# Performance work log

Measured on AMD Instinct MI355X. Metric: run time of the kernel, lower is better.

The kernel has to match this reference:

```python
import math
import jax, jax.numpy as jnp
import numpy as np

B, T, C = 4, 2048, 2048
LAYER_ID, N_LAYER = 12, 24


def setup_inputs() -> dict:
    key = jax.random.key(0)
    kx, kk, kv, kr, ko = jax.random.split(key, 5)
    x = jax.random.normal(kx, (B, T, C), dtype=jnp.float32)

    # parameter init faithful to the torch __init__
    ratio_1_to_almost0 = 1.0 - LAYER_ID / N_LAYER
    ratio_0_to_1 = LAYER_ID / (N_LAYER - 1)
    h = np.arange(C, dtype=np.float64)
    zigzag = (((np.arange(C) + 1) % 3) - 1) * 0.5
    time_first = jnp.asarray(np.ones(C) * math.log(0.3) + zigzag, dtype=jnp.float32)
    base = (h / C)  # x[0,0,i] = i / n_embed
    time_mix_k = jnp.asarray((base ** ratio_1_to_almost0)[None, None, :], dtype=jnp.float32)
    time_mix_v = jnp.asarray((base ** ratio_1_to_almost0 + 0.3 * ratio_0_to_1)[None, None, :], dtype=jnp.float32)
    time_mix_r = jnp.asarray((base ** (0.5 * ratio_1_to_almost0))[None, None, :], dtype=jnp.float32)
    xx = jnp.ones((1, 1, C), dtype=jnp.float32)
    aa = jnp.ones((1, 1, C), dtype=jnp.float32)
    bb = jnp.ones((1, 1, C), dtype=jnp.float32)
    pp = jnp.full((1, 1, C), -1e30, dtype=jnp.float32)

    scale = 0.02
    w_key = jax.random.normal(kk, (C, C), dtype=jnp.float32) * scale
    w_value = jax.random.normal(kv, (C, C), dtype=jnp.float32) * scale
    w_rec = jax.random.normal(kr, (C, C), dtype=jnp.float32) * scale
    w_out = jax.random.normal(ko, (C, C), dtype=jnp.float32) * scale

    return {"x": x, "time_first": time_first, "time_mix_k": time_mix_k,
            "time_mix_v": time_mix_v, "time_mix_r": time_mix_r,
            "xx": xx, "aa": aa, "bb": bb, "pp": pp,
            "w_key": w_key, "w_value": w_value, "w_rec": w_rec, "w_out": w_out}


def reference(x, time_first, time_mix_k, time_mix_v, time_mix_r,
              xx, aa, bb, pp, w_key, w_value, w_rec, w_out):
    # token-mix against the (constant) xx state, broadcast over (B,T)
    xk = x * time_mix_k + (1.0 - time_mix_k) * xx
    xv = x * time_mix_v + (1.0 - time_mix_v) * xx
    xr = x * time_mix_r + (1.0 - time_mix_r) * xx

    # nn.Linear(bias=False): y = x @ W^T
    k = jnp.einsum('btc,oc->bto', xk, w_key)
    v = jnp.einsum('btc,oc->bto', xv, w_value)
    r = jax.nn.sigmoid(jnp.einsum('btc,oc->bto', xr, w_rec))

    t = x.shape[1]
    # F.pad(state, (0,0, 0,t-1, 0,0)) -> (1, T, C), zeros for t > 0
    aa_p = jnp.pad(aa, ((0, 0), (0, t - 1), (0, 0)))
    bb_p = jnp.pad(bb, ((0, 0), (0, t - 1), (0, 0)))
    pp_p = jnp.pad(pp, ((0, 0), (0, t - 1), (0, 0)))

    ww = time_first + k                      # (B,T,C)
    qq = jnp.maximum(pp_p, ww)
    e1 = jnp.exp(pp_p - qq)
    e2 = jnp.exp(ww - qq)
    wkv = (e1 * aa_p + e2 * v) / (e1 * bb_p + e2)

    return jnp.einsum('btc,oc->bto', r * wkv, w_out)
```

## Files before the change

kernel.cpp:

```cpp
#include <hip/hip_runtime.h>
#include <hip/hip_bf16.h>
#include <cstdint>
#include <cstddef>

using bf16    = __bf16;
using bf16x8  = __attribute__((ext_vector_type(8))) __bf16;
using floatx4 = __attribute__((ext_vector_type(4))) float;


__device__ __forceinline__ void async_cp16(const bf16* g, bf16* l) {
    __builtin_amdgcn_global_load_lds(
        (__attribute__((address_space(1))) void*)const_cast<bf16*>(g),
        (__attribute__((address_space(3))) void*)l,
        16, 0, 0);
}

__global__ __launch_bounds__(256) void prep_cvt(
    const float* __restrict__ x, const float* __restrict__ tmv,
    const float* __restrict__ tmr, const float* __restrict__ xxp,
    const float* __restrict__ w0, const float* __restrict__ w1,
    const float* __restrict__ w2, bf16* __restrict__ xv, bf16* __restrict__ xr,
    bf16* __restrict__ o0, bf16* __restrict__ o1, bf16* __restrict__ o2,
    int C, int prepRows) {
    const int t = threadIdx.x;
    const int p = t >> 6, l = t & 63;
    const int c0 = blockIdx.x << 7;
    const int k = c0 + (p << 5) + ((l >> 4) << 3);
    const int yb = blockIdx.y;
    const int C4 = C >> 4;

    if (yb < prepRows) {
        const int r0 = yb << 4;
        const int row = r0 + (l & 15);
        const float4* xi = (const float4*)&x[(size_t)row * C + k];
        float4 a0 = xi[0], a1 = xi[1];
        float4 mv0 = *(const float4*)&tmv[k], mv1 = *(const float4*)&tmv[k + 4];
        float4 mr0 = *(const float4*)&tmr[k], mr1 = *(const float4*)&tmr[k + 4];
        float4 x00 = *(const float4*)&xxp[k], x01 = *(const float4*)&xxp[k + 4];
        float xa[8]  = {a0.x, a0.y, a0.z, a0.w, a1.x, a1.y, a1.z, a1.w};
        float mva[8] = {mv0.x, mv0.y, mv0.z, mv0.w, mv1.x, mv1.y, mv1.z, mv1.w};
        float mra[8] = {mr0.x, mr0.y, mr0.z, mr0.w, mr1.x, mr1.y, mr1.z, mr1.w};
        float x0a[8] = {x00.x, x00.y, x00.z, x00.w, x01.x, x01.y, x01.z, x01.w};
        bf16x8 ov, og;
#pragma unroll
        for (int u = 0; u < 8; ++u) {
            ov[u] = (bf16)(xa[u] * mva[u] + (1.0f - mva[u]) * x0a[u]);
            og[u] = (bf16)(xa[u] * mra[u] + (1.0f - mra[u]) * x0a[u]);
        }
        const size_t off = ((size_t)(r0 >> 4) * (C >> 5) + (c0 >> 5) + p) * 512 + l * 8;
        *(bf16x8*)&xv[off] = ov;
        *(bf16x8*)&xr[off] = og;
    } else {
        int z = yb - prepRows;
        const float* wsrc;
        bf16* wdst;
        if (z < C4) {
            wsrc = w0; wdst = o0;
        } else if (z < 2 * C4) {
            wsrc = w1; wdst = o1; z -= C4;
        } else {
            wsrc = w2; wdst = o2; z -= 2 * C4;
        }
        const int r0 = z << 4;
        const int row = r0 + (l & 15);
        const float4* wi = (const float4*)&wsrc[(size_t)row * C + k];
        float4 a0 = wi[0], a1 = wi[1];
        float wa[8] = {a0.x, a0.y, a0.z, a0.w, a1.x, a1.y, a1.z, a1.w};
        bf16x8 ov;
#pragma unroll
        for (int u = 0; u < 8; ++u) ov[u] = (bf16)wa[u];
        const size_t off = ((size_t)(r0 >> 4) * (C >> 5) + (c0 >> 5) + p) * 512 + l * 8;
        *(bf16x8*)&wdst[off] = ov;
    }
}

__global__ __launch_bounds__(256, 2) void gemm_vr(
    const bf16* __restrict__ XV, const bf16* __restrict__ XR,
    const bf16* __restrict__ WV, const bf16* __restrict__ WR,
    bf16* __restrict__ RW, int M, int N, int K) {
    __shared__ __align__(16) bf16 sXV[8192];
    __shared__ __align__(16) bf16 sXR[8192];
    __shared__ __align__(16) bf16 sWV[8192];
    __shared__ __align__(16) bf16 sWR[8192];

    const int bid = blockIdx.x;
    const int xcd = bid & 7;
    const int tt  = bid >> 3;
    const int mt  = xcd * 8 + (tt & 7);
    const int nt  = tt >> 3;

    const int tid  = threadIdx.x;
    const int wave = tid >> 6;
    const int lane = tid & 63;
    const int quad = lane >> 4;
    const int l16  = lane & 15;
    const int m0   = mt * 128;
    const int n0   = nt * 128;
    const int wm   = (wave >> 1) * 64;
    const int wn   = (wave & 1) * 64;
    const int KS   = K >> 5;

    floatx4 accv[4][4], accr[4][4];
#pragma unroll
    for (int i = 0; i < 4; ++i)
#pragma unroll
        for (int j = 0; j < 4; ++j) {
            accv[i][j] = (floatx4){0.f, 0.f, 0.f, 0.f};
            accr[i][j] = (floatx4){0.f, 0.f, 0.f, 0.f};
        }

    const size_t aoff = ((size_t)((m0 >> 4) + wave) * KS) * 512 + lane * 8;
    const size_t boff = ((size_t)((n0 >> 4) + wave) * KS) * 512 + lane * 8;
    const size_t step4 = (size_t)4 * KS * 512;
    const bf16* gXV0 = XV + aoff;
    const bf16* gXR0 = XR + aoff;
    const bf16* gWV0 = WV + boff;
    const bf16* gWR0 = WR + boff;

    const int d0 = (wave * 2) * 512;
    const int d1 = ((wave + 4) * 2) * 512;
    const int rba = (wave >> 1) * 4;
    const int rbb = (wave & 1) * 4;

    const int iters = K >> 6;
    for (int it = 0; it < iters; ++it) {
        __syncthreads();
        async_cp16(gXV0,                &sXV[d0]);
        async_cp16(gXV0 + 512,          &sXV[d0 + 512]);
        async_cp16(gXV0 + step4,        &sXV[d1]);
        async_cp16(gXV0 + step4 + 512,  &sXV[d1 + 512]);
        async_cp16(gXR0,                &sXR[d0]);
        async_cp16(gXR0 + 512,          &sXR[d0 + 512]);
        async_cp16(gXR0 + step4,        &sXR[d1]);
        async_cp16(gXR0 + step4 + 512,  &sXR[d1 + 512]);
        async_cp16(gWV0,                &sWV[d0]);
        async_cp16(gWV0 + 512,          &sWV[d0 + 512]);
        async_cp16(gWV0 + step4,        &sWV[d1]);
        async_cp16(gWV0 + step4 + 512,  &sWV[d1 + 512]);
        async_cp16(gWR0,                &sWR[d0]);
        async_cp16(gWR0 + 512,          &sWR[d0 + 512]);
        async_cp16(gWR0 + step4,        &sWR[d1]);
        async_cp16(gWR0 + step4 + 512,  &sWR[d1 + 512]);
        gXV0 += 1024; gXR0 += 1024; gWV0 += 1024; gWR0 += 1024;
        __syncthreads();

#pragma unroll
        for (int s = 0; s < 2; ++s) {
            bf16x8 av[4], bv[4];
#pragma unroll
            for (int i = 0; i < 4; ++i)
                av[i] = *(const bf16x8*)&sXV[((rba + i) * 2 + s) * 512 + (lane << 3)];
#pragma unroll
            for (int j = 0; j < 4; ++j)
                bv[j] = *(const bf16x8*)&sWV[((rbb + j) * 2 + s) * 512 + (lane << 3)];
#pragma unroll
            for (int i = 0; i < 4; ++i)
#pragma unroll
                for (int j = 0; j < 4; ++j)
                    accv[i][j] = __builtin_amdgcn_mfma_f32_16x16x32_bf16(
                        av[i], bv[j], accv[i][j], 0, 0, 0);
            bf16x8 ar[4], br[4];
#pragma unroll
            for (int i = 0; i < 4; ++i)
                ar[i] = *(const bf16x8*)&sXR[((rba + i) * 2 + s) * 512 + (lane << 3)];
#pragma unroll
            for (int j = 0; j < 4; ++j)
                br[j] = *(const bf16x8*)&sWR[((rbb + j) * 2 + s) * 512 + (lane << 3)];
#pragma unroll
            for (int i = 0; i < 4; ++i)
#pragma unroll
                for (int j = 0; j < 4; ++j)
                    accr[i][j] = __builtin_amdgcn_mfma_f32_16x16x32_bf16(
                        ar[i], br[j], accr[i][j], 0, 0, 0);
        }
    }

    const int rbase = quad * 4;
#pragma unroll
    for (int i = 0; i < 4; ++i) {
        const int rbg = ((m0 + wm) >> 4) + i;
#pragma unroll
        for (int j = 0; j < 4; ++j) {
            const int col = n0 + wn + j * 16 + l16;
            const size_t base = ((size_t)rbg * (N >> 5) + (col >> 5)) * 512 +
                                (size_t)(((col >> 3) & 3) << 4) * 8 + (col & 7);
#pragma unroll
            for (int r = 0; r < 4; ++r) {
                const float sg = 1.0f / (1.0f + __expf(-accr[i][j][r]));
                RW[base + (size_t)(rbase + r) * 8] = (bf16)(sg * accv[i][j][r]);
            }
        }
    }
}

__global__ __launch_bounds__(256, 2) void gemm_o(
    const bf16* __restrict__ A, const bf16* __restrict__ Bw,
    float* __restrict__ Of, int M, int N, int K) {
    __shared__ __align__(16) bf16 sA[8192];
    __shared__ __align__(16) bf16 sB[16384];

    const int bid = blockIdx.x;
    const int xcd = bid & 7;
    const int tt  = bid >> 3;
    const int mt  = xcd * 8 + (tt & 7);
    const int nt  = tt >> 3;

    const int tid  = threadIdx.x;
    const int wave = tid >> 6;
    const int lane = tid & 63;
    const int quad = lane >> 4;
    const int l16  = lane & 15;
    const int m0   = mt * 128;
    const int n0   = nt * 256;
    const int wm   = (wave >> 1) * 64;
    const int wnb  = (wave & 1) * 128;
    const int KS   = K >> 5;

    floatx4 acc[4][8];
#pragma unroll
    for (int i = 0; i < 4; ++i)
#pragma unroll
        for (int j = 0; j < 8; ++j) acc[i][j] = (floatx4){0.f, 0.f, 0.f, 0.f};

    const size_t step4 = (size_t)4 * KS * 512;
    const bf16* gA0 = A + ((size_t)((m0 >> 4) + wave) * KS) * 512 + lane * 8;
    const bf16* gB0 = Bw + ((size_t)((n0 >> 4) + wave) * KS) * 512 + lane * 8;
    const int dA0 = (wave * 2) * 512;
    const int dA1 = ((wave + 4) * 2) * 512;
    const int rba = (wave >> 1) * 4;
    const int rbb = (wave & 1) * 8;

    const int iters = K >> 6;
    for (int it = 0; it < iters; ++it) {
        __syncthreads();
        async_cp16(gA0,               &sA[dA0]);
        async_cp16(gA0 + 512,         &sA[dA0 + 512]);
        async_cp16(gA0 + step4,       &sA[dA1]);
        async_cp16(gA0 + step4 + 512, &sA[dA1 + 512]);
#pragma unroll
        for (int u = 0; u < 4; ++u) {
            const int dB = ((wave + 4 * u) * 2) * 512;
            async_cp16(gB0 + u * step4,       &sB[dB]);
            async_cp16(gB0 + u * step4 + 512, &sB[dB + 512]);
        }
        gA0 += 1024; gB0 += 1024;
        __syncthreads();

#pragma unroll
        for (int s = 0; s < 2; ++s) {
            bf16x8 af[4], bfg[8];
#pragma unroll
            for (int i = 0; i < 4; ++i)
                af[i] = *(const bf16x8*)&sA[((rba + i) * 2 + s) * 512 + (lane << 3)];
#pragma unroll
            for (int j = 0; j < 8; ++j)
                bfg[j] = *(const bf16x8*)&sB[((rbb + j) * 2 + s) * 512 + (lane << 3)];
#pragma unroll
            for (int i = 0; i < 4; ++i)
#pragma unroll
                for (int j = 0; j < 8; ++j)
                    acc[i][j] = __builtin_amdgcn_mfma_f32_16x16x32_bf16(
                        af[i], bfg[j], acc[i][j], 0, 0, 0);
        }
    }

    const int rbase = quad * 4;
#pragma unroll
    for (int i = 0; i < 4; ++i) {
#pragma unroll
        for (int j = 0; j < 8; ++j) {
            const int col = n0 + wnb + j * 16 + l16;
#pragma unroll
            for (int r = 0; r < 4; ++r) {
                const int row = m0 + wm + i * 16 + rbase + r;
                Of[(size_t)row * N + col] = acc[i][j][r];
            }
        }
    }
}

template <int EPI>
__global__ __launch_bounds__(256) void gemm_swz(
    const bf16* __restrict__ A, const bf16* __restrict__ Bw,
    const bf16* __restrict__ Vaux, bf16* __restrict__ Ob,
    float* __restrict__ Of, int M, int N, int K) {
    __shared__ __align__(16) bf16 sA[128 * 32];
    __shared__ __align__(16) bf16 sB[128 * 32];

    const int tid  = threadIdx.x;
    const int wave = tid >> 6;
    const int lane = tid & 63;
    const int quad = lane >> 4;
    const int l16  = lane & 15;
    const int m0   = blockIdx.y * 128;
    const int n0   = blockIdx.x * 128;
    const int wm   = (wave >> 1) * 64;
    const int wn   = (wave & 1) * 64;
    const int kslabs = K >> 5;

    floatx4 acc[4][4];
#pragma unroll
    for (int i = 0; i < 4; ++i)
#pragma unroll
        for (int j = 0; j < 4; ++j) acc[i][j] = (floatx4){0.f, 0.f, 0.f, 0.f};

    const bf16* gA0 = A + ((size_t)((m0 >> 4) + wave) * kslabs) * 512 + lane * 8;
    const bf16* gA1 = gA0 + (size_t)4 * kslabs * 512;
    const bf16* gB0 = Bw + ((size_t)((n0 >> 4) + wave) * kslabs) * 512 + lane * 8;
    const bf16* gB1 = gB0 + (size_t)4 * kslabs * 512;
    bf16* lA0 = &sA[wave * 512];
    bf16* lA1 = &sA[2048 + wave * 512];
    bf16* lB0 = &sB[wave * 512];
    bf16* lB1 = &sB[2048 + wave * 512];

    for (int it = 0; it < kslabs; ++it) {
        __syncthreads();
        async_cp16(gA0, lA0);
        async_cp16(gA1, lA1);
        async_cp16(gB0, lB0);
        async_cp16(gB1, lB1);
        gA0 += 512; gA1 += 512; gB0 += 512; gB1 += 512;
        __syncthreads();

        bf16x8 af[4], bfg[4];
#pragma unroll
        for (int i = 0; i < 4; ++i)
            af[i] = *(const bf16x8*)&sA[(((wm >> 4) + i) << 9) + (lane << 3)];
#pragma unroll
        for (int j = 0; j < 4; ++j)
            bfg[j] = *(const bf16x8*)&sB[(((wn >> 4) + j) << 9) + (lane << 3)];
#pragma unroll
        for (int i = 0; i < 4; ++i)
#pragma unroll
            for (int j = 0; j < 4; ++j)
                acc[i][j] = __builtin_amdgcn_mfma_f32_16x16x32_bf16(
                    af[i], bfg[j], acc[i][j], 0, 0, 0);
    }

    const int rbase = quad * 4;
#pragma unroll
    for (int i = 0; i < 4; ++i) {
        const int rb = ((m0 + wm) >> 4) + i;
#pragma unroll
        for (int j = 0; j < 4; ++j) {
            const int col = n0 + wn + j * 16 + l16;
            if (EPI == 2) {
#pragma unroll
                for (int r = 0; r < 4; ++r) {
                    const int row = m0 + wm + i * 16 + rbase + r;
                    Of[(size_t)row * N + col] = acc[i][j][r];
                }
            } else {
                const size_t base = ((size_t)rb * (N >> 5) + (col >> 5)) * 512 +
                                    (size_t)(((col >> 3) & 3) << 4) * 8 + (col & 7);
#pragma unroll
                for (int r = 0; r < 4; ++r) {
                    const size_t o = base + (size_t)(rbase + r) * 8;
                    const float va = acc[i][j][r];
                    if (EPI == 0) {
                        Ob[o] = (bf16)va;
                    } else {
                        const float vv = (float)Vaux[o];
                        const float sg = 1.0f / (1.0f + __expf(-va));
                        Ob[o] = (bf16)(sg * vv);
                    }
                }
            }
        }
    }
}

extern "C" void kernel_launch(void* const* d_in, const int* in_sizes, int n_in,
                              void* d_out, int out_size, void* d_ws, size_t ws_size,
                              hipStream_t stream) {
    const int C = in_sizes[1];
    const int M = in_sizes[0] / C;
    const size_t MC = (size_t)M * C;
    const size_t CC = (size_t)C * C;

    const float* x   = (const float*)d_in[0];
    const float* tmv = (const float*)d_in[3];
    const float* tmr = (const float*)d_in[4];
    const float* xxp = (const float*)d_in[5];
    const float* wv  = (const float*)d_in[10];
    const float* wr  = (const float*)d_in[11];
    const float* wo  = (const float*)d_in[12];
    float* out = (float*)d_out;

    uint8_t* ws = (uint8_t*)d_ws;
    const size_t need_full = MC * 6 + CC * 6;
    const int prepRows = M / 16;
    dim3 gridP(C / 128, M / 16 + 3 * (C / 16));

    if (ws_size >= need_full) {
        bf16* xv   = (bf16*)(ws);
        bf16* xr   = (bf16*)(ws + MC * 2);
        bf16* rwkv = (bf16*)(ws + MC * 4);
        bf16* wvb  = (bf16*)(ws + MC * 6);
        bf16* wrb  = (bf16*)(ws + MC * 6 + CC * 2);
        bf16* wob  = (bf16*)(ws + MC * 6 + CC * 4);

        prep_cvt<<<gridP, 256, 0, stream>>>(x, tmv, tmr, xxp, wv, wr, wo,
                                            xv, xr, wvb, wrb, wob, C, prepRows);
        gemm_vr<<<(M / 128) * (C / 128), 256, 0, stream>>>(xv, xr, wvb, wrb, rwkv,
                                                           M, C, C);
        gemm_o<<<(M / 128) * (C / 256), 256, 0, stream>>>(rwkv, wob, out, M, C, C);
    } else {
        bf16* xv   = (bf16*)(ws);
        bf16* xr   = (bf16*)(ws + MC * 2);
        bf16* vbuf = (bf16*)d_out;
        bf16* wvb  = (bf16*)(ws + MC * 4);
        bf16* wrb  = (bf16*)(ws + MC * 4 + CC * 2);
        bf16* wob  = (bf16*)(ws + MC * 4 + CC * 4);
        bf16* rwkv = xv;

        dim3 gridG(C / 128, M / 128);
        prep_cvt<<<gridP, 256, 0, stream>>>(x, tmv, tmr, xxp, wv, wr, wo,
                                            xv, xr, wvb, wrb, wob, C, prepRows);
        gemm_swz<0><<<gridG, 256, 0, stream>>>(xv, wvb, nullptr, vbuf, nullptr, M, C, C);
        gemm_swz<1><<<gridG, 256, 0, stream>>>(xr, wrb, vbuf, rwkv, nullptr, M, C, C);
        gemm_swz<2><<<gridG, 256, 0, stream>>>(rwkv, wob, nullptr, nullptr, out, M, C, C);
    }
}
```

Baseline: 379.3 us.

## Fold token-mix into weights and pipeline GEMMs with 4-stage LDS ring

The per-channel time-mix scaling is moved into the V and R weight matrices, and the constant xx term becomes a per-output bias computed during weight conversion. The activation is therefore converted to bf16 once instead of twice, and the fused V/R GEMM shares a single X tile. Both GEMMs move to 512-thread blocks with 256-row tiles and a 4-slot async LDS ring buffer with explicit waitcnt, barriers and setprio to overlap loads with MFMA. The fallback path for small workspaces is dropped, so the kernel now returns early if the workspace is too small. Folding the mix into bf16 weights changes rounding slightly.

```diff
diff --git a/kernel.cpp b/kernel.cpp
--- a/kernel.cpp
+++ b/kernel.cpp
@@ -15,357 +15,339 @@
         16, 0, 0);
 }
 
-__global__ __launch_bounds__(256) void prep_cvt(
+template <int VM>
+__device__ __forceinline__ void wait_vm() {
+    if constexpr (VM == 8)      asm volatile("s_waitcnt vmcnt(8)" ::: "memory");
+    else if constexpr (VM == 4) asm volatile("s_waitcnt vmcnt(4)" ::: "memory");
+    else if constexpr (VM == 0) asm volatile("s_waitcnt vmcnt(0)" ::: "memory");
+}
+
+__device__ __forceinline__ void barrier_pin() {
+    __builtin_amdgcn_s_barrier();
+    __builtin_amdgcn_sched_barrier(0);
+}
+
+__global__ __launch_bounds__(256) void prep3(
     const float* __restrict__ x, const float* __restrict__ tmv,
     const float* __restrict__ tmr, const float* __restrict__ xxp,
-    const float* __restrict__ w0, const float* __restrict__ w1,
-    const float* __restrict__ w2, bf16* __restrict__ xv, bf16* __restrict__ xr,
-    bf16* __restrict__ o0, bf16* __restrict__ o1, bf16* __restrict__ o2,
+    const float* __restrict__ wv, const float* __restrict__ wr,
+    const float* __restrict__ wo, bf16* __restrict__ xb,
+    bf16* __restrict__ wvb, bf16* __restrict__ wrb, bf16* __restrict__ wob,
+    float* __restrict__ pV, float* __restrict__ pR,
     int C, int prepRows) {
-    const int t = threadIdx.x;
-    const int p = t >> 6, l = t & 63;
+    __shared__ float red[4][16];
+    const int t  = threadIdx.x;
+    const int p  = t >> 6, l = t & 63;
     const int c0 = blockIdx.x << 7;
-    const int k = c0 + (p << 5) + ((l >> 4) << 3);
+    const int k  = c0 + (p << 5) + ((l >> 4) << 3);
     const int yb = blockIdx.y;
     const int C4 = C >> 4;
 
     if (yb < prepRows) {
-        const int r0 = yb << 4;
-        const int row = r0 + (l & 15);
+        const int row = (yb << 4) + (l & 15);
         const float4* xi = (const float4*)&x[(size_t)row * C + k];
-        float4 a0 = xi[0], a1 = xi[1];
-        float4 mv0 = *(const float4*)&tmv[k], mv1 = *(const float4*)&tmv[k + 4];
-        float4 mr0 = *(const float4*)&tmr[k], mr1 = *(const float4*)&tmr[k + 4];
-        float4 x00 = *(const float4*)&xxp[k], x01 = *(const float4*)&xxp[k + 4];
-        float xa[8]  = {a0.x, a0.y, a0.z, a0.w, a1.x, a1.y, a1.z, a1.w};
-        float mva[8] = {mv0.x, mv0.y, mv0.z, mv0.w, mv1.x, mv1.y, mv1.z, mv1.w};
-        float mra[8] = {mr0.x, mr0.y, mr0.z, mr0.w, mr1.x, mr1.y, mr1.z, mr1.w};
-        float x0a[8] = {x00.x, x00.y, x00.z, x00.w, x01.x, x01.y, x01.z, x01.w};
-        bf16x8 ov, og;
-#pragma unroll
-        for (int u = 0; u < 8; ++u) {
-            ov[u] = (bf16)(xa[u] * mva[u] + (1.0f - mva[u]) * x0a[u]);
-            og[u] = (bf16)(xa[u] * mra[u] + (1.0f - mra[u]) * x0a[u]);
-        }
-        const size_t off = ((size_t)(r0 >> 4) * (C >> 5) + (c0 >> 5) + p) * 512 + l * 8;
-        *(bf16x8*)&xv[off] = ov;
-        *(bf16x8*)&xr[off] = og;
+        const float4 a0 = xi[0], a1 = xi[1];
+        const float xa[8] = {a0.x, a0.y, a0.z, a0.w, a1.x, a1.y, a1.z, a1.w};
+        bf16x8 ov;
+#pragma unroll
+        for (int u = 0; u < 8; ++u) ov[u] = (bf16)xa[u];
+        const size_t off = ((size_t)yb * (C >> 5) + (c0 >> 5) + p) * 512 + l * 8;
+        *(bf16x8*)&xb[off] = ov;
     } else {
         int z = yb - prepRows;
-        const float* wsrc;
-        bf16* wdst;
-        if (z < C4) {
-            wsrc = w0; wdst = o0;
-        } else if (z < 2 * C4) {
-            wsrc = w1; wdst = o1; z -= C4;
+        const float* wsrc; bf16* wdst; const float* sv = nullptr;
+        float* bdst = nullptr; int mix = 1;
+        if (z < C4)          { wsrc = wv; wdst = wvb; sv = tmv; bdst = pV; }
+        else if (z < 2 * C4) { wsrc = wr; wdst = wrb; sv = tmr; bdst = pR; z -= C4; }
+        else                 { wsrc = wo; wdst = wob; mix = 0; z -= 2 * C4; }
+        const int row = (z << 4) + (l & 15);
+        const float4* wi = (const float4*)&wsrc[(size_t)row * C + k];
+        const float4 b0 = wi[0], b1 = wi[1];
+        const float wa[8] = {b0.x, b0.y, b0.z, b0.w, b1.x, b1.y, b1.z, b1.w};
+        bf16x8 ov;
+        if (mix) {
+            const float4 s0 = *(const float4*)&sv[k],  s1 = *(const float4*)&sv[k + 4];
+            const float4 q0 = *(const float4*)&xxp[k], q1 = *(const float4*)&xxp[k + 4];
+            const float sa[8] = {s0.x, s0.y, s0.z, s0.w, s1.x, s1.y, s1.z, s1.w};
+            const float qa[8] = {q0.x, q0.y, q0.z, q0.w, q1.x, q1.y, q1.z, q1.w};
+            float part = 0.f;
+#pragma unroll
+            for (int u = 0; u < 8; ++u) {
+                part += (1.0f - sa[u]) * qa[u] * wa[u];
+                ov[u] = (bf16)(wa[u] * sa[u]);
+            }
+            part += __shfl_xor(part, 16);
+            part += __shfl_xor(part, 32);
+            if (l < 16) red[p][l] = part;
+            __syncthreads();
+            if (t < 16) {
+                const float s = red[0][t] + red[1][t] + red[2][t] + red[3][t];
+                bdst[(size_t)(c0 >> 7) * C + (z << 4) + t] = s;
+            }
         } else {
-            wsrc = w2; wdst = o2; z -= 2 * C4;
-        }
-        const int r0 = z << 4;
-        const int row = r0 + (l & 15);
-        const float4* wi = (const float4*)&wsrc[(size_t)row * C + k];
-        float4 a0 = wi[0], a1 = wi[1];
-        float wa[8] = {a0.x, a0.y, a0.z, a0.w, a1.x, a1.y, a1.z, a1.w};
-        bf16x8 ov;
-#pragma unroll
-        for (int u = 0; u < 8; ++u) ov[u] = (bf16)wa[u];
-        const size_t off = ((size_t)(r0 >> 4) * (C >> 5) + (c0 >> 5) + p) * 512 + l * 8;
+#pragma unroll
+            for (int u = 0; u < 8; ++u) ov[u] = (bf16)wa[u];
+        }
+        const size_t off = ((size_t)z * (C >> 5) + (c0 >> 5) + p) * 512 + l * 8;
         *(bf16x8*)&wdst[off] = ov;
     }
 }
 
-__global__ __launch_bounds__(256, 2) void gemm_vr(
-    const bf16* __restrict__ XV, const bf16* __restrict__ XR,
-    const bf16* __restrict__ WV, const bf16* __restrict__ WR,
-    bf16* __restrict__ RW, int M, int N, int K) {
-    __shared__ __align__(16) bf16 sXV[8192];
-    __shared__ __align__(16) bf16 sXR[8192];
-    __shared__ __align__(16) bf16 sWV[8192];
-    __shared__ __align__(16) bf16 sWR[8192];
-
-    const int bid = blockIdx.x;
-    const int xcd = bid & 7;
-    const int tt  = bid >> 3;
-    const int mt  = xcd * 8 + (tt & 7);
-    const int nt  = tt >> 3;
+__global__ __launch_bounds__(512, 2) void gemm_vr3(
+    const bf16* __restrict__ XB, const bf16* __restrict__ WVB,
+    const bf16* __restrict__ WRB, const float* __restrict__ pV,
+    const float* __restrict__ pR, bf16* __restrict__ RW,
+    int M, int N, int K) {
+    __shared__ __align__(16) bf16 lds[65536];
+
+    const int bid    = blockIdx.x;
+    const int xcd    = bid & 7;
+    const int tt     = bid >> 3;
+    const int mtPerX = (M >> 8) >> 3;
+    const int mt     = xcd * mtPerX + (tt % mtPerX);
+    const int nt     = tt / mtPerX;
+    const int m0     = mt << 8;
+    const int n0     = nt << 7;
 
     const int tid  = threadIdx.x;
     const int wave = tid >> 6;
     const int lane = tid & 63;
     const int quad = lane >> 4;
     const int l16  = lane & 15;
-    const int m0   = mt * 128;
-    const int n0   = nt * 128;
-    const int wm   = (wave >> 1) * 64;
-    const int wn   = (wave & 1) * 64;
+    const int wm   = (wave >> 2) << 7;
+    const int wn   = (wave & 3) << 5;
+    const int xrb  = (wave >> 2) << 3;
+    const int wjb  = (wave & 3) << 1;
     const int KS   = K >> 5;
-
-    floatx4 accv[4][4], accr[4][4];
-#pragma unroll
-    for (int i = 0; i < 4; ++i)
-#pragma unroll
-        for (int j = 0; j < 4; ++j) {
+    const int Q    = K >> 5;
+
+    const bf16* gsrc;
+    int grb, ldsOff;
+    if (wave < 4)      { gsrc = XB;  grb = (m0 >> 4) + wave * 4;       ldsOff = wave * 2048; }
+    else if (wave < 6) { gsrc = WVB; grb = (n0 >> 4) + (wave - 4) * 4; ldsOff = 8192 + (wave - 4) * 2048; }
+    else               { gsrc = WRB; grb = (n0 >> 4) + (wave - 6) * 4; ldsOff = 12288 + (wave - 6) * 2048; }
+    const size_t rstep = (size_t)KS * 512;
+    const bf16* g0 = gsrc + (size_t)grb * rstep + lane * 8;
+
+    floatx4 accv[8][2], accr[8][2];
+#pragma unroll
+    for (int i = 0; i < 8; ++i)
+#pragma unroll
+        for (int j = 0; j < 2; ++j) {
             accv[i][j] = (floatx4){0.f, 0.f, 0.f, 0.f};
             accr[i][j] = (floatx4){0.f, 0.f, 0.f, 0.f};
         }
 
-    const size_t aoff = ((size_t)((m0 >> 4) + wave) * KS) * 512 + lane * 8;
-    const size_t boff = ((size_t)((n0 >> 4) + wave) * KS) * 512 + lane * 8;
-    const size_t step4 = (size_t)4 * KS * 512;
-    const bf16* gXV0 = XV + aoff;
-    const bf16* gXR0 = XR + aoff;
-    const bf16* gWV0 = WV + boff;
-    const bf16* gWR0 = WR + boff;
-
-    const int d0 = (wave * 2) * 512;
-    const int d1 = ((wave + 4) * 2) * 512;
-    const int rba = (wave >> 1) * 4;
-    const int rbb = (wave & 1) * 4;
-
-    const int iters = K >> 6;
-    for (int it = 0; it < iters; ++it) {
-        __syncthreads();
-        async_cp16(gXV0,                &sXV[d0]);
-        async_cp16(gXV0 + 512,          &sXV[d0 + 512]);
-        async_cp16(gXV0 + step4,        &sXV[d1]);
-        async_cp16(gXV0 + step4 + 512,  &sXV[d1 + 512]);
-        async_cp16(gXR0,                &sXR[d0]);
-        async_cp16(gXR0 + 512,          &sXR[d0 + 512]);
-        async_cp16(gXR0 + step4,        &sXR[d1]);
-        async_cp16(gXR0 + step4 + 512,  &sXR[d1 + 512]);
-        async_cp16(gWV0,                &sWV[d0]);
-        async_cp16(gWV0 + 512,          &sWV[d0 + 512]);
-        async_cp16(gWV0 + step4,        &sWV[d1]);
-        async_cp16(gWV0 + step4 + 512,  &sWV[d1 + 512]);
-        async_cp16(gWR0,                &sWR[d0]);
-        async_cp16(gWR0 + 512,          &sWR[d0 + 512]);
-        async_cp16(gWR0 + step4,        &sWR[d1]);
-        async_cp16(gWR0 + step4 + 512,  &sWR[d1 + 512]);
-        gXV0 += 1024; gXR0 += 1024; gWV0 += 1024; gWR0 += 1024;
-        __syncthreads();
-
-#pragma unroll
-        for (int s = 0; s < 2; ++s) {
-            bf16x8 av[4], bv[4];
-#pragma unroll
-            for (int i = 0; i < 4; ++i)
-                av[i] = *(const bf16x8*)&sXV[((rba + i) * 2 + s) * 512 + (lane << 3)];
-#pragma unroll
-            for (int j = 0; j < 4; ++j)
-                bv[j] = *(const bf16x8*)&sWV[((rbb + j) * 2 + s) * 512 + (lane << 3)];
-#pragma unroll
-            for (int i = 0; i < 4; ++i)
-#pragma unroll
-                for (int j = 0; j < 4; ++j)
-                    accv[i][j] = __builtin_amdgcn_mfma_f32_16x16x32_bf16(
-                        av[i], bv[j], accv[i][j], 0, 0, 0);
-            bf16x8 ar[4], br[4];
-#pragma unroll
-            for (int i = 0; i < 4; ++i)
-                ar[i] = *(const bf16x8*)&sXR[((rba + i) * 2 + s) * 512 + (lane << 3)];
-#pragma unroll
-            for (int j = 0; j < 4; ++j)
-                br[j] = *(const bf16x8*)&sWR[((rbb + j) * 2 + s) * 512 + (lane << 3)];
-#pragma unroll
-            for (int i = 0; i < 4; ++i)
-#pragma unroll
-                for (int j = 0; j < 4; ++j)
-                    accr[i][j] = __builtin_amdgcn_mfma_f32_16x16x32_bf16(
-                        ar[i], br[j], accr[i][j], 0, 0, 0);
-        }
-    }
-
-    const int rbase = quad * 4;
-#pragma unroll
-    for (int i = 0; i < 4; ++i) {
-        const int rbg = ((m0 + wm) >> 4) + i;
-#pragma unroll
-        for (int j = 0; j < 4; ++j) {
-            const int col = n0 + wn + j * 16 + l16;
-            const size_t base = ((size_t)rbg * (N >> 5) + (col >> 5)) * 512 +
-                                (size_t)(((col >> 3) & 3) << 4) * 8 + (col & 7);
+    for (int s = 0; s < 3; ++s) {
+        bf16* dst = &lds[s * 16384 + ldsOff];
+        async_cp16(g0,             dst);
+        async_cp16(g0 + rstep,     dst + 512);
+        async_cp16(g0 + 2 * rstep, dst + 1024);
+        async_cp16(g0 + 3 * rstep, dst + 1536);
+        g0 += 512;
+    }
+    wait_vm<8>();
+    barrier_pin();
+
+#define VR_SLICE(q, DO_STAGE, VMEND)                                           \
+    {                                                                          \
+        const int slot = (q) & 3;                                              \
+        const bf16* sb = &lds[slot * 16384];                                   \
+        bf16x8 xf[8], wvf[2], wrf[2];                                          \
+        _Pragma("unroll")                                                      \
+        for (int i = 0; i < 8; ++i)                                            \
+            xf[i] = *(const bf16x8*)&sb[(xrb + i) * 512 + (lane << 3)];        \
+        _Pragma("unroll")                                                      \
+        for (int j = 0; j < 2; ++j)                                            \
+            wvf[j] = *(const bf16x8*)&sb[8192 + (wjb + j) * 512 + (lane << 3)];\
+        bf16* dst = &lds[(((q) + 3) & 3) * 16384 + ldsOff];                    \
+        if (DO_STAGE) {                                                        \
+            async_cp16(g0,         dst);                                       \
+            async_cp16(g0 + rstep, dst + 512);                                 \
+        }                                                                      \
+        __builtin_amdgcn_s_barrier();                                          \
+        asm volatile("s_waitcnt lgkmcnt(0)" ::: "memory");                     \
+        __builtin_amdgcn_sched_barrier(0);                                     \
+        __builtin_amdgcn_s_setprio(1);                                         \
+        _Pragma("unroll")                                                      \
+        for (int i = 0; i < 8; ++i)                                            \
+            _Pragma("unroll")                                                  \
+            for (int j = 0; j < 2; ++j)                                        \
+                accv[i][j] = __builtin_amdgcn_mfma_f32_16x16x32_bf16(          \
+                    xf[i], wvf[j], accv[i][j], 0, 0, 0);                       \
+        __builtin_amdgcn_s_setprio(0);                                         \
+        barrier_pin();                                                         \
+        _Pragma("unroll")                                                      \
+        for (int j = 0; j < 2; ++j)                                            \
+            wrf[j] = *(const bf16x8*)&sb[12288 + (wjb + j) * 512 + (lane << 3)];\
+        if (DO_STAGE) {                                                        \
+            async_cp16(g0 + 2 * rstep, dst + 1024);                            \
+            async_cp16(g0 + 3 * rstep, dst + 1536);                            \
+            g0 += 512;                                                         \
+        }                                                                      \
+        __builtin_amdgcn_s_barrier();                                          \
+        asm volatile("s_waitcnt lgkmcnt(0)" ::: "memory");                     \
+        __builtin_amdgcn_sched_barrier(0);                                     \
+        __builtin_amdgcn_s_setprio(1);                                         \
+        _Pragma("unroll")                                                      \
+        for (int i = 0; i < 8; ++i)                                            \
+            _Pragma("unroll")                                                  \
+            for (int j = 0; j < 2; ++j)                                        \
+                accr[i][j] = __builtin_amdgcn_mfma_f32_16x16x32_bf16(          \
+                    xf[i], wrf[j], accr[i][j], 0, 0, 0);                       \
+        __builtin_amdgcn_s_setprio(0);                                         \
+        wait_vm<VMEND>();                                                      \
+        barrier_pin();                                                         \
+    }
+
+    for (int q = 0; q < Q - 3; ++q) VR_SLICE(q, 1, 8)
+    VR_SLICE(Q - 3, 0, 4)
+    VR_SLICE(Q - 2, 0, 0)
+    VR_SLICE(Q - 1, 0, -1)
+#undef VR_SLICE
+
+#pragma unroll
+    for (int j = 0; j < 2; ++j) {
+        const int col = n0 + wn + j * 16 + l16;
+        float bvj = 0.f, brj = 0.f;
+#pragma unroll
+        for (int s = 0; s < 16; ++s) {
+            bvj += pV[(size_t)s * N + col];
+            brj += pR[(size_t)s * N + col];
+        }
+        const size_t cbase = (size_t)(col >> 5) * 512 +
+                             (size_t)(((col >> 3) & 3) << 4) * 8 + (col & 7);
+#pragma unroll
+        for (int i = 0; i < 8; ++i) {
+            const int rbg = ((m0 + wm) >> 4) + i;
+            const size_t base = (size_t)rbg * (N >> 5) * 512 + cbase;
 #pragma unroll
             for (int r = 0; r < 4; ++r) {
-                const float sg = 1.0f / (1.0f + __expf(-accr[i][j][r]));
-                RW[base + (size_t)(rbase + r) * 8] = (bf16)(sg * accv[i][j][r]);
+                const float vv = accv[i][j][r] + bvj;
+                const float rr = accr[i][j][r] + brj;
+                const float sg = 1.0f / (1.0f + __expf(-rr));
+                RW[base + (size_t)(quad * 4 + r) * 8] = (bf16)(sg * vv);
             }
         }
     }
 }
 
-__global__ __launch_bounds__(256, 2) void gemm_o(
-    const bf16* __restrict__ A, const bf16* __restrict__ Bw,
+__global__ __launch_bounds__(512, 2) void gemm_o3(
+    const bf16* __restrict__ AB, const bf16* __restrict__ WB,
     float* __restrict__ Of, int M, int N, int K) {
-    __shared__ __align__(16) bf16 sA[8192];
-    __shared__ __align__(16) bf16 sB[16384];
-
-    const int bid = blockIdx.x;
-    const int xcd = bid & 7;
-    const int tt  = bid >> 3;
-    const int mt  = xcd * 8 + (tt & 7);
-    const int nt  = tt >> 3;
+    __shared__ __align__(16) bf16 lds[65536];
+
+    const int bid    = blockIdx.x;
+    const int xcd    = bid & 7;
+    const int tt     = bid >> 3;
+    const int mtPerX = (M >> 8) >> 3;
+    const int mt     = xcd * mtPerX + (tt % mtPerX);
+    const int nt     = tt / mtPerX;
+    const int m0     = mt << 8;
+    const int n0     = nt << 8;
 
     const int tid  = threadIdx.x;
     const int wave = tid >> 6;
     const int lane = tid & 63;
     const int quad = lane >> 4;
     const int l16  = lane & 15;
-    const int m0   = mt * 128;
-    const int n0   = nt * 256;
-    const int wm   = (wave >> 1) * 64;
-    const int wnb  = (wave & 1) * 128;
+    const int wm   = (wave >> 2) << 7;
+    const int wn   = (wave & 3) << 6;
+    const int xrb  = (wave >> 2) << 3;
+    const int wjb  = (wave & 3) << 2;
     const int KS   = K >> 5;
-
-    floatx4 acc[4][8];
-#pragma unroll
-    for (int i = 0; i < 4; ++i)
-#pragma unroll
-        for (int j = 0; j < 8; ++j) acc[i][j] = (floatx4){0.f, 0.f, 0.f, 0.f};
-
-    const size_t step4 = (size_t)4 * KS * 512;
-    const bf16* gA0 = A + ((size_t)((m0 >> 4) + wave) * KS) * 512 + lane * 8;
-    const bf16* gB0 = Bw + ((size_t)((n0 >> 4) + wave) * KS) * 512 + lane * 8;
-    const int dA0 = (wave * 2) * 512;
-    const int dA1 = ((wave + 4) * 2) * 512;
-    const int rba = (wave >> 1) * 4;
-    const int rbb = (wave & 1) * 8;
-
-    const int iters = K >> 6;
-    for (int it = 0; it < iters; ++it) {
-        __syncthreads();
-        async_cp16(gA0,               &sA[dA0]);
-        async_cp16(gA0 + 512,         &sA[dA0 + 512]);
-        async_cp16(gA0 + step4,       &sA[dA1]);
-        async_cp16(gA0 + step4 + 512, &sA[dA1 + 512]);
-#pragma unroll
-        for (int u = 0; u < 4; ++u) {
-            const int dB = ((wave + 4 * u) * 2) * 512;
-            async_cp16(gB0 + u * step4,       &sB[dB]);
-            async_cp16(gB0 + u * step4 + 512, &sB[dB + 512]);
-        }
-        gA0 += 1024; gB0 += 1024;
-        __syncthreads();
-
-#pragma unroll
-        for (int s = 0; s < 2; ++s) {
-            bf16x8 af[4], bfg[8];
-#pragma unroll
-            for (int i = 0; i < 4; ++i)
-                af[i] = *(const bf16x8*)&sA[((rba + i) * 2 + s) * 512 + (lane << 3)];
-#pragma unroll
-            for (int j = 0; j < 8; ++j)
-                bfg[j] = *(const bf16x8*)&sB[((rbb + j) * 2 + s) * 512 + (lane << 3)];
-#pragma unroll
-            for (int i = 0; i < 4; ++i)
-#pragma unroll
-                for (int j = 0; j < 8; ++j)
-                    acc[i][j] = __builtin_amdgcn_mfma_f32_16x16x32_bf16(
-                        af[i], bfg[j], acc[i][j], 0, 0, 0);
-        }
-    }
-
-    const int rbase = quad * 4;
-#pragma unroll
-    for (int i = 0; i < 4; ++i) {
-#pragma unroll
-        for (int j = 0; j < 8; ++j) {
-            const int col = n0 + wnb + j * 16 + l16;
-#pragma unroll
-            for (int r = 0; r < 4; ++r) {
-                const int row = m0 + wm + i * 16 + rbase + r;
-                Of[(size_t)row * N + col] = acc[i][j][r];
-            }
-        }
-    }
-}
-
-template <int EPI>
-__global__ __launch_bounds__(256) void gemm_swz(
-    const bf16* __restrict__ A, const bf16* __restrict__ Bw,
-    const bf16* __restrict__ Vaux, bf16* __restrict__ Ob,
-    float* __restrict__ Of, int M, int N, int K) {
-    __shared__ __align__(16) bf16 sA[128 * 32];
-    __shared__ __align__(16) bf16 sB[128 * 32];
-
-    const int tid  = threadIdx.x;
-    const int wave = tid >> 6;
-    const int lane = tid & 63;
-    const int quad = lane >> 4;
-    const int l16  = lane & 15;
-    const int m0   = blockIdx.y * 128;
-    const int n0   = blockIdx.x * 128;
-    const int wm   = (wave >> 1) * 64;
-    const int wn   = (wave & 1) * 64;
-    const int kslabs = K >> 5;
-
-    floatx4 acc[4][4];
-#pragma unroll
-    for (int i = 0; i < 4; ++i)
+    const int Q    = K >> 5;
+
+    const bf16* gsrc;
+    int grb, ldsOff;
+    if (wave < 4) { gsrc = AB; grb = (m0 >> 4) + wave * 4;       ldsOff = wave * 2048; }
+    else          { gsrc = WB; grb = (n0 >> 4) + (wave - 4) * 4; ldsOff = 8192 + (wave - 4) * 2048; }
+    const size_t rstep = (size_t)KS * 512;
+    const bf16* g0 = gsrc + (size_t)grb * rstep + lane * 8;
+
+    floatx4 acc[8][4];
+#pragma unroll
+    for (int i = 0; i < 8; ++i)
 #pragma unroll
         for (int j = 0; j < 4; ++j) acc[i][j] = (floatx4){0.f, 0.f, 0.f, 0.f};
 
-    const bf16* gA0 = A + ((size_t)((m0 >> 4) + wave) * kslabs) * 512 + lane * 8;
-    const bf16* gA1 = gA0 + (size_t)4 * kslabs * 512;
-    const bf16* gB0 = Bw + ((size_t)((n0 >> 4) + wave) * kslabs) * 512 + lane * 8;
-    const bf16* gB1 = gB0 + (size_t)4 * kslabs * 512;
-    bf16* lA0 = &sA[wave * 512];
-    bf16* lA1 = &sA[2048 + wave * 512];
-    bf16* lB0 = &sB[wave * 512];
-    bf16* lB1 = &sB[2048 + wave * 512];
-
-    for (int it = 0; it < kslabs; ++it) {
-        __syncthreads();
-        async_cp16(gA0, lA0);
-        async_cp16(gA1, lA1);
-        async_cp16(gB0, lB0);
-        async_cp16(gB1, lB1);
-        gA0 += 512; gA1 += 512; gB0 += 512; gB1 += 512;
-        __syncthreads();
-
-        bf16x8 af[4], bfg[4];
-#pragma unroll
-        for (int i = 0; i < 4; ++i)
-            af[i] = *(const bf16x8*)&sA[(((wm >> 4) + i) << 9) + (lane << 3)];
-#pragma unroll
-        for (int j = 0; j < 4; ++j)
-            bfg[j] = *(const bf16x8*)&sB[(((wn >> 4) + j) << 9) + (lane << 3)];
-#pragma unroll
-        for (int i = 0; i < 4; ++i)
-#pragma unroll
-            for (int j = 0; j < 4; ++j)
-                acc[i][j] = __builtin_amdgcn_mfma_f32_16x16x32_bf16(
-                    af[i], bfg[j], acc[i][j], 0, 0, 0);
-    }
-
-    const int rbase = quad * 4;
-#pragma unroll
-    for (int i = 0; i < 4; ++i) {
-        const int rb = ((m0 + wm) >> 4) + i;
+    for (int s = 0; s < 3; ++s) {
+        bf16* dst = &lds[s * 16384 + ldsOff];
+        async_cp16(g0,             dst);
+        async_cp16(g0 + rstep,     dst + 512);
+        async_cp16(g0 + 2 * rstep, dst + 1024);
+        async_cp16(g0 + 3 * rstep, dst + 1536);
+        g0 += 512;
+    }
+    wait_vm<8>();
+    barrier_pin();
+
+#define O_SLICE(q, DO_STAGE, VMEND)                                            \
+    {                                                                          \
+        const int slot = (q) & 3;                                              \
+        const bf16* sb = &lds[slot * 16384];                                   \
+        bf16x8 xf[8], wf[4];                                                   \
+        _Pragma("unroll")                                                      \
+        for (int i = 0; i < 8; ++i)                                            \
+            xf[i] = *(const bf16x8*)&sb[(xrb + i) * 512 + (lane << 3)];        \
+        _Pragma("unroll")                                                      \
+        for (int j = 0; j < 2; ++j)                                            \
+            wf[j] = *(const bf16x8*)&sb[8192 + (wjb + j) * 512 + (lane << 3)]; \
+        bf16* dst = &lds[(((q) + 3) & 3) * 16384 + ldsOff];                    \
+        if (DO_STAGE) {                                                        \
+            async_cp16(g0,         dst);                                       \
+            async_cp16(g0 + rstep, dst + 512);                                 \
+        }                                                                      \
+        __builtin_amdgcn_s_barrier();                                          \
+        asm volatile("s_waitcnt lgkmcnt(0)" ::: "memory");                     \
+        __builtin_amdgcn_sched_barrier(0);                                     \
+        __builtin_amdgcn_s_setprio(1);                                         \
+        _Pragma("unroll")                                                      \
+        for (int i = 0; i < 8; ++i)                                            \
+            _Pragma("unroll")                                                  \
+            for (int j = 0; j < 2; ++j)                                        \
+                acc[i][j] = __builtin_amdgcn_mfma_f32_16x16x32_bf16(           \
+                    xf[i], wf[j], acc[i][j], 0, 0, 0);                         \
+        __builtin_amdgcn_s_setprio(0);                                         \
+        barrier_pin();                                                         \
+        _Pragma("unroll")                                                      \
+        for (int j = 2; j < 4; ++j)                                            \
+            wf[j] = *(const bf16x8*)&sb[8192 + (wjb + j) * 512 + (lane << 3)]; \
+        if (DO_STAGE) {                                                        \
+            async_cp16(g0 + 2 * rstep, dst + 1024);                            \
+            async_cp16(g0 + 3 * rstep, dst + 1536);                            \
+            g0 += 512;                                                         \
+        }                                                                      \
+        __builtin_amdgcn_s_barrier();                                          \
+        asm volatile("s_waitcnt lgkmcnt(0)" ::: "memory");                     \
+        __builtin_amdgcn_sched_barrier(0);                                     \
+        __builtin_amdgcn_s_setprio(1);                                         \
+        _Pragma("unroll")                                                      \
+        for (int i = 0; i < 8; ++i)                                            \
+            _Pragma("unroll")                                                  \
+            for (int j = 2; j < 4; ++j)                                        \
+                acc[i][j] = __builtin_amdgcn_mfma_f32_16x16x32_bf16(           \
+                    xf[i], wf[j], acc[i][j], 0, 0, 0);                         \
+        __builtin_amdgcn_s_setprio(0);                                         \
+        wait_vm<VMEND>();                                                      \
+        barrier_pin();                                                         \
+    }
+
+    for (int q = 0; q < Q - 3; ++q) O_SLICE(q, 1, 8)
+    O_SLICE(Q - 3, 0, 4)
+    O_SLICE(Q - 2, 0, 0)
+    O_SLICE(Q - 1, 0, -1)
+#undef O_SLICE
+
+#pragma unroll
+    for (int i = 0; i < 8; ++i) {
+        const int row0 = m0 + wm + i * 16 + quad * 4;
 #pragma unroll
         for (int j = 0; j < 4; ++j) {
             const int col = n0 + wn + j * 16 + l16;
-            if (EPI == 2) {
-#pragma unroll
-                for (int r = 0; r < 4; ++r) {
-                    const int row = m0 + wm + i * 16 + rbase + r;
-                    Of[(size_t)row * N + col] = acc[i][j][r];
-                }
-            } else {
-                const size_t base = ((size_t)rb * (N >> 5) + (col >> 5)) * 512 +
-                                    (size_t)(((col >> 3) & 3) << 4) * 8 + (col & 7);
-#pragma unroll
-                for (int r = 0; r < 4; ++r) {
-                    const size_t o = base + (size_t)(rbase + r) * 8;
-                    const float va = acc[i][j][r];
-                    if (EPI == 0) {
-                        Ob[o] = (bf16)va;
-                    } else {
-                        const float vv = (float)Vaux[o];
-                        const float sg = 1.0f / (1.0f + __expf(-va));
-                        Ob[o] = (bf16)(sg * vv);
-                    }
-                }
-            }
+#pragma unroll
+            for (int r = 0; r < 4; ++r)
+                Of[(size_t)(row0 + r) * N + col] = acc[i][j][r];
         }
     }
 }
@@ -385,40 +367,23 @@
     const float* wv  = (const float*)d_in[10];
     const float* wr  = (const float*)d_in[11];
     const float* wo  = (const float*)d_in[12];
-    float* out = (float*)d_out;
 
     uint8_t* ws = (uint8_t*)d_ws;
-    const size_t need_full = MC * 6 + CC * 6;
-    const int prepRows = M / 16;
+    bf16* xb    = (bf16*)ws;
+    bf16* rwkv  = (bf16*)(ws + MC * 2);
+    bf16* wvb   = (bf16*)(ws + MC * 4);
+    bf16* wrb   = (bf16*)(ws + MC * 4 + CC * 2);
+    bf16* wob   = (bf16*)(ws + MC * 4 + CC * 4);
+    float* pV   = (float*)(ws + MC * 4 + CC * 6);
+    float* pR   = pV + 16 * (size_t)C;
+    const size_t need = MC * 4 + CC * 6 + (size_t)C * 128;
+    if (ws_size < need) return;
+
     dim3 gridP(C / 128, M / 16 + 3 * (C / 16));
-
-    if (ws_size >= need_full) {
-        bf16* xv   = (bf16*)(ws);
-        bf16* xr   = (bf16*)(ws + MC * 2);
-        bf16* rwkv = (bf16*)(ws + MC * 4);
-        bf16* wvb  = (bf16*)(ws + MC * 6);
-        bf16* wrb  = (bf16*)(ws + MC * 6 + CC * 2);
-        bf16* wob  = (bf16*)(ws + MC * 6 + CC * 4);
-
-        prep_cvt<<<gridP, 256, 0, stream>>>(x, tmv, tmr, xxp, wv, wr, wo,
-                                            xv, xr, wvb, wrb, wob, C, prepRows);
-        gemm_vr<<<(M / 128) * (C / 128), 256, 0, stream>>>(xv, xr, wvb, wrb, rwkv,
-                                                           M, C, C);
-        gemm_o<<<(M / 128) * (C / 256), 256, 0, stream>>>(rwkv, wob, out, M, C, C);
-    } else {
-        bf16* xv   = (bf16*)(ws);
-        bf16* xr   = (bf16*)(ws + MC * 2);
-        bf16* vbuf = (bf16*)d_out;
-        bf16* wvb  = (bf16*)(ws + MC * 4);
-        bf16* wrb  = (bf16*)(ws + MC * 4 + CC * 2);
-        bf16* wob  = (bf16*)(ws + MC * 4 + CC * 4);
-        bf16* rwkv = xv;
-
-        dim3 gridG(C / 128, M / 128);
-        prep_cvt<<<gridP, 256, 0, stream>>>(x, tmv, tmr, xxp, wv, wr, wo,
-                                            xv, xr, wvb, wrb, wob, C, prepRows);
-        gemm_swz<0><<<gridG, 256, 0, stream>>>(xv, wvb, nullptr, vbuf, nullptr, M, C, C);
-        gemm_swz<1><<<gridG, 256, 0, stream>>>(xr, wrb, vbuf, rwkv, nullptr, M, C, C);
-        gemm_swz<2><<<gridG, 256, 0, stream>>>(rwkv, wob, nullptr, nullptr, out, M, C, C);
-    }
-}
+    prep3<<<gridP, 256, 0, stream>>>(x, tmv, tmr, xxp, wv, wr, wo,
+                                     xb, wvb, wrb, wob, pV, pR, C, M / 16);
+    gemm_vr3<<<(M / 256) * (C / 128), 512, 0, stream>>>(xb, wvb, wrb, pV, pR,
+                                                        rwkv, M, C, C);
+    gemm_o3<<<(M / 256) * (C / 256), 512, 0, stream>>>(rwkv, wob, (float*)d_out,
+                                                       M, C, C);
+}
```

New measurement: 353.9 us. 6.7% less time.
